# Performance work log

Measured on AMD Instinct MI355X. Metric: run time of the kernel, lower is better.

The kernel has to match this reference:

```python
import jax, jax.numpy as jnp
import numpy as np

N, IN, H, C = 100000, 128, 4, 64  # nodes, in_channels, heads, out_channels
E0 = 1600000
NEG_SLOPE = 0.2


def setup_inputs() -> dict:
    key = jax.random.key(0)
    ks = jax.random.split(key, 8)
    x = jax.random.normal(ks[0], (N, IN), dtype=jnp.float32)
    edge_index = jax.random.randint(ks[1], (2, E0), 0, N, dtype=jnp.int64)
    s = 1.0 / np.sqrt(IN)
    W = jax.random.uniform(ks[2], (IN, H * C), jnp.float32, -s, s)
    att_src = jax.random.normal(ks[3], (H, C), jnp.float32) * 0.1
    att_dst = jax.random.normal(ks[4], (H, C), jnp.float32) * 0.1
    bias = jnp.zeros((C,), jnp.float32)
    sf = 1.0 / np.sqrt(C)
    fc_w = jax.random.uniform(ks[5], (C, 1), jnp.float32, -sf, sf)
    fc_b = jax.random.uniform(ks[6], (1,), jnp.float32, -sf, sf)
    return {"x": x, "edge_index": edge_index, "W": W, "att_src": att_src,
            "att_dst": att_dst, "bias": bias, "fc_w": fc_w, "fc_b": fc_b}


def gat_forward(x, edge_index, W, att_src, att_dst, bias, fc_w, fc_b):
    n = x.shape[0]
    # add self-loops (PyG GATConv default)
    loops = jnp.arange(n, dtype=edge_index.dtype)
    src = jnp.concatenate([edge_index[0], loops])
    dst = jnp.concatenate([edge_index[1], loops])

    h = (x @ W).reshape(n, H, C)                     # [N,H,C]
    a_src = jnp.einsum('nhc,hc->nh', h, att_src)     # [N,H]
    a_dst = jnp.einsum('nhc,hc->nh', h, att_dst)

    logits = jax.nn.leaky_relu(a_src[src] + a_dst[dst], NEG_SLOPE)  # [E,H]
    m = jax.ops.segment_max(logits, dst, num_segments=n)            # [N,H]
    e = jnp.exp(logits - m[dst])
    z = jax.ops.segment_sum(e, dst, num_segments=n)                 # [N,H]
    alpha = e / (z[dst] + 1e-16)                                    # [E,H]

    msgs = h[src] * alpha[:, :, None]                               # [E,H,C]
    out = jax.ops.segment_sum(msgs, dst, num_segments=n)            # [N,H,C]
    out = out.mean(axis=1) + bias                                   # concat=False -> head mean

    out = jax.nn.relu(out)
    return jax.nn.sigmoid(out @ fc_w + fc_b)                        # [N,1]


def reference(x, edge_index, W, att_src, att_dst, bias, fc_w, fc_b):
    return gat_forward(x, edge_index, W, att_src, att_dst, bias, fc_w, fc_b)
```

## Files before the change

### kernel.cpp

```cpp
#include <hip/hip_runtime.h>


#define NN 100000
#define IN_DIM 128
#define HC 256
#define NEG_SLOPE 0.2f
#define SLOTS 96

typedef __attribute__((ext_vector_type(8))) __bf16 bf16x8;
typedef __attribute__((ext_vector_type(4))) float f32x4;
typedef __attribute__((ext_vector_type(2))) float f32x2;

__global__ __launch_bounds__(256, 4) void k_gemm(const float* __restrict__ x,
    const float* __restrict__ W, const float* __restrict__ att_src,
    const float* __restrict__ att_dst, unsigned char* __restrict__ h8,
    float* __restrict__ a_src, float* __restrict__ a_dst,
    int* __restrict__ cnt, int n_tiles) {
  const int tid = threadIdx.x;
  { int gti = blockIdx.x * 256 + tid; if (gti < NN) cnt[gti] = 0; }
  const int cg = blockIdx.x & 3;
  const int rblk = blockIdx.x >> 2;
  const int wave = tid >> 6, lane = tid & 63;
  const int g = lane >> 4, i16 = lane & 15;

  bf16x8 wf[4][4];
  float as_l[4], ad_l[4];
  #pragma unroll
  for (int nt = 0; nt < 4; ++nt) {
    const int col = cg * 64 + nt * 16 + i16;
    as_l[nt] = att_src[col];
    ad_l[nt] = att_dst[col];
    #pragma unroll
    for (int kk = 0; kk < 4; ++kk) {
      const float* wp = W + (size_t)(kk * 32 + g * 8) * HC + col;
      bf16x8 f;
      #pragma unroll
      for (int j = 0; j < 8; ++j) f[j] = (__bf16)wp[(size_t)j * HC];
      wf[nt][kk] = f;
    }
  }

  for (int t = rblk; t < n_tiles; t += 256) {
    const int rbase = t * 64 + wave * 16;
    int arow = rbase + i16; if (arow >= NN) arow = NN - 1;
    const float* xp = x + (size_t)arow * IN_DIM;
    f32x4 acc[4];
    #pragma unroll
    for (int nt = 0; nt < 4; ++nt) acc[nt] = (f32x4){0.f, 0.f, 0.f, 0.f};
    #pragma unroll
    for (int kk = 0; kk < 4; ++kk) {
      const int k0 = kk * 32 + g * 8;
      f32x4 xa = *(const f32x4*)(xp + k0);
      f32x4 xb = *(const f32x4*)(xp + k0 + 4);
      bf16x8 af;
      af[0] = (__bf16)xa[0]; af[1] = (__bf16)xa[1];
      af[2] = (__bf16)xa[2]; af[3] = (__bf16)xa[3];
      af[4] = (__bf16)xb[0]; af[5] = (__bf16)xb[1];
      af[6] = (__bf16)xb[2]; af[7] = (__bf16)xb[3];
      #pragma unroll
      for (int nt = 0; nt < 4; ++nt)
        acc[nt] = __builtin_amdgcn_mfma_f32_16x16x32_bf16(af, wf[nt][kk], acc[nt], 0, 0, 0);
    }
    float ps[4] = {0.f, 0.f, 0.f, 0.f}, pd[4] = {0.f, 0.f, 0.f, 0.f};
    #pragma unroll
    for (int nt = 0; nt < 4; ++nt) {
      #pragma unroll
      for (int r = 0; r < 4; ++r) {
        ps[r] += acc[nt][r] * as_l[nt];
        pd[r] += acc[nt][r] * ad_l[nt];
      }
    }
    #pragma unroll
    for (int r = 0; r < 4; ++r) {
      #pragma unroll
      for (int d = 1; d <= 8; d <<= 1) {
        ps[r] += __shfl_xor(ps[r], d);
        pd[r] += __shfl_xor(pd[r], d);
      }
      const int row = rbase + g * 4 + r;
      if (row < NN) {
        if (i16 == 0) {
          a_src[(size_t)row * 4 + cg] = ps[r];
          a_dst[(size_t)row * 4 + cg] = pd[r];
        }
        unsigned char* hp = h8 + (size_t)row * HC + cg * 64 + i16;
        #pragma unroll
        for (int nt = 0; nt < 4; ++nt) {
          unsigned int pv = __builtin_amdgcn_cvt_pk_fp8_f32(acc[nt][r], acc[nt][r], 0, false);
          hp[nt * 16] = (unsigned char)pv;
        }
      }
    }
  }
}

__global__ void k_scatter(const int* __restrict__ ei, int* __restrict__ cnt,
                          int* __restrict__ csr, int e0) {
  int e = blockIdx.x * 256 + threadIdx.x;
  if (e >= e0) return;
  int s = ei[e], d = ei[e0 + e];
  int p = atomicAdd(&cnt[d], 1);
  if (p < SLOTS) csr[(size_t)d * SLOTS + p] = s;
}

__global__ __launch_bounds__(256) void k_main(const unsigned char* __restrict__ h8,
    const float* __restrict__ a_src, const float* __restrict__ a_dst,
    const int* __restrict__ cnt, const int* __restrict__ csr,
    const float* __restrict__ bias, const float* __restrict__ fc_w,
    const float* __restrict__ fc_b, float* __restrict__ out, int n0) {
  const int tid = threadIdx.x, lane = tid & 63;
  const int n = n0 + blockIdx.x * 4 + (tid >> 6);
  if (n >= NN) return;
  const int eh = lane >> 5;
  const int c8 = lane & 31;
  const int head = c8 >> 3;
  const float wz = ((c8 & 7) == 0) ? 1.f : 0.f;
  const unsigned char* __restrict__ hb = h8 + c8 * 8;
  const float adh = a_dst[n * 4 + head];
  const int beg = n * SLOTS;
  int ne = cnt[n]; if (ne > SLOTS) ne = SLOTS;
  const int end = beg + ne;

  float a0, a1, a2, a3, a4, a5, a6, a7, zl;
  {
    float lg = a_src[n * 4 + head] + adh;
    lg = fmaxf(lg, NEG_SLOPE * lg);
    const float ev = (eh == 0) ? __expf(lg) : 0.f;
    zl = wz * ev;
    const uint2 hv = *(const uint2*)(hb + ((size_t)n << 8));
    const f32x2 f01 = __builtin_amdgcn_cvt_pk_f32_fp8(hv.x, false);
    const f32x2 f23 = __builtin_amdgcn_cvt_pk_f32_fp8(hv.x, true);
    const f32x2 f45 = __builtin_amdgcn_cvt_pk_f32_fp8(hv.y, false);
    const f32x2 f67 = __builtin_amdgcn_cvt_pk_f32_fp8(hv.y, true);
    a0 = ev * f01[0]; a1 = ev * f01[1];
    a2 = ev * f23[0]; a3 = ev * f23[1];
    a4 = ev * f45[0]; a5 = ev * f45[1];
    a6 = ev * f67[0]; a7 = ev * f67[1];
  }

  int b0 = beg;
  const int bend = beg + (ne & ~7);
  for (; b0 < bend; b0 += 8) {
    #pragma unroll
    for (int u = 0; u < 4; ++u) {
      const int sv = csr[b0 + u * 2 + eh];
      float lg = a_src[sv * 4 + head] + adh;
      lg = fmaxf(lg, NEG_SLOPE * lg);
      const float ev = __expf(lg);
      zl += wz * ev;
      const uint2 hv = *(const uint2*)(hb + ((size_t)sv << 8));
      const f32x2 f01 = __builtin_amdgcn_cvt_pk_f32_fp8(hv.x, false);
      const f32x2 f23 = __builtin_amdgcn_cvt_pk_f32_fp8(hv.x, true);
      const f32x2 f45 = __builtin_amdgcn_cvt_pk_f32_fp8(hv.y, false);
      const f32x2 f67 = __builtin_amdgcn_cvt_pk_f32_fp8(hv.y, true);
      a0 += ev * f01[0]; a1 += ev * f01[1];
      a2 += ev * f23[0]; a3 += ev * f23[1];
      a4 += ev * f45[0]; a5 += ev * f45[1];
      a6 += ev * f67[0]; a7 += ev * f67[1];
    }
  }
  for (; b0 < end; b0 += 2) {
    const int idx = b0 + eh;
    const bool v = idx < end;
    const int sv = csr[v ? idx : beg];
    float lg = a_src[sv * 4 + head] + adh;
    lg = fmaxf(lg, NEG_SLOPE * lg);
    float ev = v ? __expf(lg) : 0.f;
    zl += wz * ev;
    const uint2 hv = *(const uint2*)(hb + ((size_t)sv << 8));
    const f32x2 f01 = __builtin_amdgcn_cvt_pk_f32_fp8(hv.x, false);
    const f32x2 f23 = __builtin_amdgcn_cvt_pk_f32_fp8(hv.x, true);
    const f32x2 f45 = __builtin_amdgcn_cvt_pk_f32_fp8(hv.y, false);
    const f32x2 f67 = __builtin_amdgcn_cvt_pk_f32_fp8(hv.y, true);
    a0 += ev * f01[0]; a1 += ev * f01[1];
    a2 += ev * f23[0]; a3 += ev * f23[1];
    a4 += ev * f45[0]; a5 += ev * f45[1];
    a6 += ev * f67[0]; a7 += ev * f67[1];
  }
  a0 += __shfl_xor(a0, 32); a1 += __shfl_xor(a1, 32);
  a2 += __shfl_xor(a2, 32); a3 += __shfl_xor(a3, 32);
  a4 += __shfl_xor(a4, 32); a5 += __shfl_xor(a5, 32);
  a6 += __shfl_xor(a6, 32); a7 += __shfl_xor(a7, 32);
  zl += __shfl_xor(zl, 32);
  zl += __shfl_xor(zl, 1); zl += __shfl_xor(zl, 2); zl += __shfl_xor(zl, 4);
  const float rz = 0.25f / (zl + 1e-16f);
  a0 *= rz; a1 *= rz; a2 *= rz; a3 *= rz;
  a4 *= rz; a5 *= rz; a6 *= rz; a7 *= rz;
  a0 += __shfl_xor(a0, 8); a0 += __shfl_xor(a0, 16);
  a1 += __shfl_xor(a1, 8); a1 += __shfl_xor(a1, 16);
  a2 += __shfl_xor(a2, 8); a2 += __shfl_xor(a2, 16);
  a3 += __shfl_xor(a3, 8); a3 += __shfl_xor(a3, 16);
  a4 += __shfl_xor(a4, 8); a4 += __shfl_xor(a4, 16);
  a5 += __shfl_xor(a5, 8); a5 += __shfl_xor(a5, 16);
  a6 += __shfl_xor(a6, 8); a6 += __shfl_xor(a6, 16);
  a7 += __shfl_xor(a7, 8); a7 += __shfl_xor(a7, 16);

  const int ch0 = (c8 & 7) * 8;
  const f32x4 bv0 = *(const f32x4*)(bias + ch0);
  const f32x4 bv1 = *(const f32x4*)(bias + ch0 + 4);
  const f32x4 wv0 = *(const f32x4*)(fc_w + ch0);
  const f32x4 wv1 = *(const f32x4*)(fc_w + ch0 + 4);
  float p = fmaxf(a0 + bv0[0], 0.f) * wv0[0] + fmaxf(a1 + bv0[1], 0.f) * wv0[1]
          + fmaxf(a2 + bv0[2], 0.f) * wv0[2] + fmaxf(a3 + bv0[3], 0.f) * wv0[3]
          + fmaxf(a4 + bv1[0], 0.f) * wv1[0] + fmaxf(a5 + bv1[1], 0.f) * wv1[1]
          + fmaxf(a6 + bv1[2], 0.f) * wv1[2] + fmaxf(a7 + bv1[3], 0.f) * wv1[3];
  p += __shfl_xor(p, 1); p += __shfl_xor(p, 2); p += __shfl_xor(p, 4);
  if (lane == 0) out[n] = 1.f / (1.f + __expf(-(p + fc_b[0])));
}

extern "C" void kernel_launch(void* const* d_in, const int* in_sizes, int n_in,
                              void* d_out, int out_size, void* d_ws, size_t ws_size,
                              hipStream_t stream) {
  const float* x       = (const float*)d_in[0];
  const int*   ei      = (const int*)d_in[1];
  const float* W       = (const float*)d_in[2];
  const float* att_src = (const float*)d_in[3];
  const float* att_dst = (const float*)d_in[4];
  const float* bias    = (const float*)d_in[5];
  const float* fc_w    = (const float*)d_in[6];
  const float* fc_b    = (const float*)d_in[7];
  float* out = (float*)d_out;
  const int e0 = in_sizes[1] / 2;

  char* ws = (char*)d_ws;
  size_t off = 0;
  auto carve = [&](size_t bytes) {
    void* p = ws + off;
    off = (off + bytes + 255) & ~(size_t)255;
    return p;
  };
  unsigned char* h8 = (unsigned char*)carve((size_t)NN * HC);
  float* a_src = (float*)carve((size_t)NN * 4 * 4);
  float* a_dst = (float*)carve((size_t)NN * 4 * 4);
  int* cnt     = (int*)carve((size_t)NN * 4);
  int* csrbuf  = (int*)carve((size_t)NN * SLOTS * 4);

  const int n_tiles = (NN + 63) / 64;
  k_gemm<<<dim3(1024), dim3(256), 0, stream>>>(x, W, att_src, att_dst,
                                               h8, a_src, a_dst, cnt, n_tiles);
  k_scatter<<<dim3((e0 + 255) / 256), dim3(256), 0, stream>>>(ei, cnt, csrbuf, e0);
  const int third = 8334;
  k_main<<<dim3(third), dim3(256), 0, stream>>>(h8, a_src, a_dst, cnt, csrbuf,
                                                bias, fc_w, fc_b, out, 0);
  k_main<<<dim3(third), dim3(256), 0, stream>>>(h8, a_src, a_dst, cnt, csrbuf,
                                                bias, fc_w, fc_b, out, 33336);
  k_main<<<dim3(8333), dim3(256), 0, stream>>>(h8, a_src, a_dst, cnt, csrbuf,
                                               bias, fc_w, fc_b, out, 66672);
}
```

Baseline: 319.1 us.

## Build exact CSR via two-level counting sort instead of fixed-slot atomic buckets

Replaces the single atomic scatter into fixed 96-slot per-node buckets with a multi-pass counting sort. Per-block histograms over 64-node buckets are column-scanned and block-scanned to get offsets, edges are scattered into bucket order, and each bucket is sorted locally to produce a compact CSR with rowptr. This removes the truncation at 96 edges and global atomics contention, and gives k_main a dense, contiguous edge list. The cost is five extra kernel launches, an 8-byte-per-edge intermediate buffer, and several more passes over edge data.

```diff
diff --git a/kernel.cpp b/kernel.cpp
--- a/kernel.cpp
+++ b/kernel.cpp
@@ -5,7 +5,8 @@
 #define IN_DIM 128
 #define HC 256
 #define NEG_SLOPE 0.2f
-#define SLOTS 96
+#define NB 1563
+#define HB 128
 
 typedef __attribute__((ext_vector_type(8))) __bf16 bf16x8;
 typedef __attribute__((ext_vector_type(4))) float f32x4;
@@ -14,10 +15,8 @@
 __global__ __launch_bounds__(256, 4) void k_gemm(const float* __restrict__ x,
     const float* __restrict__ W, const float* __restrict__ att_src,
     const float* __restrict__ att_dst, unsigned char* __restrict__ h8,
-    float* __restrict__ a_src, float* __restrict__ a_dst,
-    int* __restrict__ cnt, int n_tiles) {
+    float* __restrict__ a_src, float* __restrict__ a_dst, int n_tiles) {
   const int tid = threadIdx.x;
-  { int gti = blockIdx.x * 256 + tid; if (gti < NN) cnt[gti] = 0; }
   const int cg = blockIdx.x & 3;
   const int rblk = blockIdx.x >> 2;
   const int wave = tid >> 6, lane = tid & 63;
@@ -94,18 +93,106 @@
   }
 }
 
-__global__ void k_scatter(const int* __restrict__ ei, int* __restrict__ cnt,
-                          int* __restrict__ csr, int e0) {
-  int e = blockIdx.x * 256 + threadIdx.x;
-  if (e >= e0) return;
-  int s = ei[e], d = ei[e0 + e];
-  int p = atomicAdd(&cnt[d], 1);
-  if (p < SLOTS) csr[(size_t)d * SLOTS + p] = s;
+__global__ __launch_bounds__(256) void k_hist(const int* __restrict__ ei,
+    int* __restrict__ bh, int e0, int ch) {
+  __shared__ int h[NB];
+  const int b = blockIdx.x, tid = threadIdx.x;
+  for (int k = tid; k < NB; k += 256) h[k] = 0;
+  __syncthreads();
+  const int lo = b * ch, hi = min(lo + ch, e0);
+  for (int e = lo + tid; e < hi; e += 256)
+    atomicAdd(&h[((unsigned)ei[e0 + e]) >> 6], 1);
+  __syncthreads();
+  for (int k = tid; k < NB; k += 256) bh[(size_t)b * NB + k] = h[k];
+}
+
+__global__ __launch_bounds__(256) void k_colscan(int* __restrict__ bh,
+                                                 int* __restrict__ total) {
+  int k = blockIdx.x * 256 + threadIdx.x;
+  if (k >= NB) return;
+  int run = 0;
+  for (int b = 0; b < HB; ++b) {
+    size_t i = (size_t)b * NB + k;
+    int t = bh[i]; bh[i] = run; run += t;
+  }
+  total[k] = run;
+}
+
+__global__ __launch_bounds__(256) void k_bscan(const int* __restrict__ total,
+                                               int* __restrict__ base, int e0) {
+  __shared__ int ls[256];
+  const int t = threadIdx.x;
+  int vals[7]; int lsum = 0;
+  #pragma unroll
+  for (int i = 0; i < 7; ++i) {
+    int k = t * 7 + i;
+    vals[i] = (k < NB) ? total[k] : 0;
+    lsum += vals[i];
+  }
+  ls[t] = lsum; __syncthreads();
+  for (int off = 1; off < 256; off <<= 1) {
+    int v = (t >= off) ? ls[t - off] : 0;
+    __syncthreads(); ls[t] += v; __syncthreads();
+  }
+  int excl = (t == 0) ? 0 : ls[t - 1];
+  #pragma unroll
+  for (int i = 0; i < 7; ++i) {
+    int k = t * 7 + i;
+    if (k < NB) base[k] = excl;
+    excl += vals[i];
+  }
+  if (t == 255) base[NB] = e0;
+}
+
+__global__ __launch_bounds__(256) void k_scat(const int* __restrict__ ei,
+    const int* __restrict__ bh, const int* __restrict__ base,
+    uint2* __restrict__ rec, int e0, int ch) {
+  __shared__ int cur[NB];
+  const int b = blockIdx.x, tid = threadIdx.x;
+  for (int k = tid; k < NB; k += 256)
+    cur[k] = base[k] + bh[(size_t)b * NB + k];
+  __syncthreads();
+  const int lo = b * ch, hi = min(lo + ch, e0);
+  for (int e = lo + tid; e < hi; e += 256) {
+    int s = ei[e], d = ei[e0 + e];
+    int p = atomicAdd(&cur[((unsigned)d) >> 6], 1);
+    rec[p] = (uint2){(unsigned)d, (unsigned)s};
+  }
+}
+
+__global__ __launch_bounds__(256) void k_bsort(const uint2* __restrict__ rec,
+    const int* __restrict__ base, int* __restrict__ csr,
+    int* __restrict__ rowptr, int e0) {
+  __shared__ int cnt64[64], pre[64];
+  const int k = blockIdx.x, tid = threadIdx.x;
+  const int lo = base[k], hi = base[k + 1];
+  if (tid < 64) cnt64[tid] = 0;
+  __syncthreads();
+  for (int i = lo + tid; i < hi; i += 256)
+    atomicAdd(&cnt64[rec[i].x & 63], 1);
+  __syncthreads();
+  if (tid == 0) {
+    int run = 0;
+    for (int j = 0; j < 64; ++j) { pre[j] = run; run += cnt64[j]; }
+  }
+  __syncthreads();
+  if (tid < 64) {
+    int n = k * 64 + tid;
+    if (n < NN) rowptr[n] = lo + pre[tid];
+    cnt64[tid] = lo + pre[tid];
+  }
+  if (k == NB - 1 && tid == 0) rowptr[NN] = e0;
+  __syncthreads();
+  for (int i = lo + tid; i < hi; i += 256) {
+    uint2 r = rec[i];
+    int p = atomicAdd(&cnt64[r.x & 63], 1);
+    csr[p] = (int)r.y;
+  }
 }
 
 __global__ __launch_bounds__(256) void k_main(const unsigned char* __restrict__ h8,
     const float* __restrict__ a_src, const float* __restrict__ a_dst,
-    const int* __restrict__ cnt, const int* __restrict__ csr,
+    const int* __restrict__ rowptr, const int* __restrict__ csr,
     const float* __restrict__ bias, const float* __restrict__ fc_w,
     const float* __restrict__ fc_b, float* __restrict__ out, int n0) {
   const int tid = threadIdx.x, lane = tid & 63;
@@ -117,9 +204,9 @@
   const float wz = ((c8 & 7) == 0) ? 1.f : 0.f;
   const unsigned char* __restrict__ hb = h8 + c8 * 8;
   const float adh = a_dst[n * 4 + head];
-  const int beg = n * SLOTS;
-  int ne = cnt[n]; if (ne > SLOTS) ne = SLOTS;
-  const int end = beg + ne;
+  const int beg = rowptr[n];
+  const int end = rowptr[n + 1];
+  const int ne = end - beg;
 
   float a0, a1, a2, a3, a4, a5, a6, a7, zl;
   {
@@ -232,18 +319,27 @@
   unsigned char* h8 = (unsigned char*)carve((size_t)NN * HC);
   float* a_src = (float*)carve((size_t)NN * 4 * 4);
   float* a_dst = (float*)carve((size_t)NN * 4 * 4);
-  int* cnt     = (int*)carve((size_t)NN * 4);
-  int* csrbuf  = (int*)carve((size_t)NN * SLOTS * 4);
+  int* bh      = (int*)carve((size_t)HB * NB * 4);
+  int* total   = (int*)carve((size_t)NB * 4);
+  int* base    = (int*)carve((size_t)(NB + 1) * 4);
+  int* rowptr  = (int*)carve((size_t)(NN + 1) * 4);
+  uint2* rec   = (uint2*)carve((size_t)e0 * 8);
+  int* csrbuf  = (int*)carve((size_t)e0 * 4);
 
   const int n_tiles = (NN + 63) / 64;
+  const int ch = (e0 + HB - 1) / HB;
   k_gemm<<<dim3(1024), dim3(256), 0, stream>>>(x, W, att_src, att_dst,
-                                               h8, a_src, a_dst, cnt, n_tiles);
-  k_scatter<<<dim3((e0 + 255) / 256), dim3(256), 0, stream>>>(ei, cnt, csrbuf, e0);
+                                               h8, a_src, a_dst, n_tiles);
+  k_hist<<<dim3(HB), dim3(256), 0, stream>>>(ei, bh, e0, ch);
+  k_colscan<<<dim3((NB + 255) / 256), dim3(256), 0, stream>>>(bh, total);
+  k_bscan<<<dim3(1), dim3(256), 0, stream>>>(total, base, e0);
+  k_scat<<<dim3(HB), dim3(256), 0, stream>>>(ei, bh, base, rec, e0, ch);
+  k_bsort<<<dim3(NB), dim3(256), 0, stream>>>(rec, base, csrbuf, rowptr, e0);
   const int third = 8334;
-  k_main<<<dim3(third), dim3(256), 0, stream>>>(h8, a_src, a_dst, cnt, csrbuf,
+  k_main<<<dim3(third), dim3(256), 0, stream>>>(h8, a_src, a_dst, rowptr, csrbuf,
                                                 bias, fc_w, fc_b, out, 0);
-  k_main<<<dim3(third), dim3(256), 0, stream>>>(h8, a_src, a_dst, cnt, csrbuf,
+  k_main<<<dim3(third), dim3(256), 0, stream>>>(h8, a_src, a_dst, rowptr, csrbuf,
                                                 bias, fc_w, fc_b, out, 33336);
-  k_main<<<dim3(8333), dim3(256), 0, stream>>>(h8, a_src, a_dst, cnt, csrbuf,
+  k_main<<<dim3(8333), dim3(256), 0, stream>>>(h8, a_src, a_dst, rowptr, csrbuf,
                                                bias, fc_w, fc_b, out, 66672);
 }
```

Measured after the change: 322.4 us. Within noise of the previous version (+1.0%).
